# Optimization experiments

Hardware: AMD Instinct MI355X
Metric: run time of the kernel (lower is better)

Reference implementation:

```python
import jax, jax.numpy as jnp
from jax import lax
import numpy as np

B, N = 8192, 4096


def thomas_algorithm(a, b, c, f):
    """Batched Thomas tridiagonal solve.
    a: (B, N-1) sub-diagonal (row i uses a[:, i-1])
    b: (B, N)   diagonal
    c: (B, N-1) super-diagonal (row i uses c[:, i])
    f: (B, N)   rhs
    returns u: (B, N) with A u = f
    """
    Bb = f.shape[0]
    zero_col = jnp.zeros((Bb, 1), dtype=f.dtype)
    a_full = jnp.concatenate([zero_col, a], axis=1)  # (B, N), a_full[:,0] unused (=0)
    c_full = jnp.concatenate([c, zero_col], axis=1)  # (B, N), c_full[:,N-1] unused (=0)

    def fwd_step(carry, inp):
        cp_prev, dp_prev = carry
        ai, bi, ci, fi = inp
        denom = bi - ai * cp_prev
        cp = ci / denom
        dp = (fi - ai * dp_prev) / denom
        return (cp, dp), (cp, dp)

    init = (jnp.zeros(Bb, dtype=f.dtype), jnp.zeros(Bb, dtype=f.dtype))
    xs = (a_full.T, b.T, c_full.T, f.T)  # scan over N, vectorized over B
    _, (cps, dps) = lax.scan(fwd_step, init, xs)

    def bwd_step(u_next, inp):
        cp, dp = inp
        u = dp - cp * u_next
        return u, u

    _, us = lax.scan(bwd_step, jnp.zeros(Bb, dtype=f.dtype), (cps, dps), reverse=True)
    return us.T  # (B, N)


def setup_inputs() -> dict:
    key = jax.random.key(0)
    k1, k2 = jax.random.split(key)
    alpha = jax.random.uniform(k1, (B, N), dtype=jnp.float32)
    f = jax.random.normal(k2, (N,), dtype=jnp.float32)
    return {"alpha": alpha, "f": f}


def reference(alpha, f):
    # f is 1D metadata -> expand to batch, matching torch forward
    f2 = jnp.broadcast_to(f[None, :], alpha.shape)
    # tridiagonal_matrix(alpha)
    a = alpha[:, :-1] ** 2
    b = jnp.maximum(5.0 + alpha ** 3, 0.01)
    c = alpha[:, 1:] ** 2 + 2.0 * alpha[:, 1:]
    u = thomas_algorithm(a, b, c, f2)
    return u
```

## Files before the change

kernel.cpp:

```cpp
#include <hip/hip_runtime.h>


namespace {
constexpr int kN   = 4096;
constexpr int kCH  = 32;
constexpr int kHL  = 8;
constexpr int kR   = kCH + kHL;
constexpr int kNC  = kN / kCH;
constexpr int RPW  = 8;
constexpr int WAVES = 2;
constexpr int THREADS = 64 * WAVES;
constexpr int F4PR = 76;
constexpr int ST4  = 77;
constexpr int APW4 = RPW * ST4;
constexpr int SF4  = 141;
}

__global__ __launch_bounds__(THREADS) void thomas_v7(
    const float4* __restrict__ alpha4,
    const float4* __restrict__ f4,
    float4* __restrict__ u4)
{
  __shared__ float4 sM[WAVES * APW4 + SF4];

  const int bid  = blockIdx.x;
  const int pair = bid & 7;
  const int r0   = (bid >> 3) * (WAVES * RPW);
  const int w    = threadIdx.x >> 6;
  const int lane = threadIdx.x & 63;
  const int rw0  = r0 + w * RPW;
  const int j    = lane & 7;
  const int q    = lane >> 3;

  float4* __restrict__ sA = sM + w * APW4;
  float4* __restrict__ sF = sM + WAVES * APW4;

#define LOAD_TILE(cw, P)                                              \
  {                                                                   \
    const int cb4 = (cw) * 64 - 3;                                    \
    _Pragma("unroll")                                                 \
    for (int it = 0; it < 10; ++it) {                                 \
      int idx = lane + it * 64;                                       \
      if (idx > RPW * F4PR - 1) idx = RPW * F4PR - 1;        \
      const int row = idx / F4PR;                                     \
      const int c4  = idx - row * F4PR;                               \
      int g4 = cb4 + c4;                                              \
      g4 = (g4 < 0) ? 0 : ((g4 > 1023) ? 1023 : g4);   \
      P[it] = alpha4[(size_t)(rw0 + row) * 1024 + g4];                \
    }                                                                 \
  }

#define WRITE_TILE(P)                                                 \
  {                                                                   \
    _Pragma("unroll")                                                 \
    for (int it = 0; it < 10; ++it) {                                 \
      const int idx = lane + it * 64;                                 \
      if (idx < RPW * F4PR) {                                         \
        const int row = idx / F4PR;                                   \
        const int c4  = idx - row * F4PR;                             \
        sA[row * ST4 + c4] = P[it];                                   \
      }                                                               \
    }                                                                 \
  }

#define STEP(am1v, fiv)                                        \
  {                                                            \
    const float c_  = ap1 * (ap1 + 2.0f);                      \
    const float b_  = fmaxf(fmaf(a0 * a0, a0, 5.0f), 0.01f);   \
    const float dn  = fmaf(-c_, ec, b_);                       \
    const float rd  = __builtin_amdgcn_rcpf(dn);               \
    gc = (fiv - c_ * gc) * rd;                                 \
    ec = ((am1v) * (am1v)) * rd;                               \
    ap1 = a0; a0 = (am1v);                                     \
  }

#define SOLVE_TILE(CWL)                                                   \
  {                                                                       \
    const int  kk    = (pair * 2 + (CWL)) * 8 + q;                        \
    const bool first = (kk == 0);                                         \
    const bool last  = (kk == kNC - 1);                                   \
    const int  f4b   = first ? 3 : (q * 8 + 1);                           \
    const int  fOff  = (CWL) * 64;                                        \
    const float4* __restrict__ A4 = sA + j * ST4;                         \
    float gp[kR], ep[kR];                                                 \
    float ec = 0.0f, gc = 0.0f, ap1 = 0.0f;                               \
    const int ghi = last ? 9 : 17;                                        \
    float4 curA = A4[f4b + ghi];                                          \
    float4 lowA = A4[f4b + ghi - 1];                                      \
    float4 fcur = sF[fOff + f4b + ghi];                                   \
    float4 flow = sF[fOff + f4b + ghi - 1];                               \
    float a0 = curA.w;                                                    \
    if (!last) {                                                          \
      _Pragma("unroll")                                                   \
      for (int g = 17; g >= 10; --g) {                                    \
        const float4 pA = A4[f4b + g - 2];                                \
        const float4 pF = sF[fOff + f4b + g - 2];                         \
        STEP(curA.z, fcur.w)                                              \
        STEP(curA.y, fcur.z)                                              \
        STEP(curA.x, fcur.y)                                              \
        STEP(lowA.w, fcur.x)                                              \
        curA = lowA; lowA = pA; fcur = flow; flow = pF;                   \
      }                                                                   \
    }                                                                     \
    _Pragma("unroll")                                                     \
    for (int g = 9; g >= 0; --g) {                                        \
      int pidx = f4b + g - 2;                                             \
      if (pidx < 0) pidx = 0;              \
      const float4 pA = A4[pidx];                                         \
      const float4 pF = sF[fOff + pidx];                                  \
      float lw = lowA.w;                                                  \
      if (g == 0 && first) lw = 0.0f;                        \
      STEP(curA.z, fcur.w)  gp[4*g+3] = gc; ep[4*g+3] = ec;               \
      STEP(curA.y, fcur.z)  gp[4*g+2] = gc; ep[4*g+2] = ec;               \
      STEP(curA.x, fcur.y)  gp[4*g+1] = gc; ep[4*g+1] = ec;               \
      STEP(lw,     fcur.x)  gp[4*g+0] = gc; ep[4*g+0] = ec;               \
      curA = lowA; lowA = pA; fcur = flow; flow = pF;                     \
    }                                                                     \
    const int tmin = first ? 0 : kHL;                                     \
    float up = 0.0f;                                                      \
    float4 pk;                                                            \
    _Pragma("unroll")                                                     \
    for (int t = 0; t < kR; ++t) {                                        \
      const float uv = fmaf(-ep[t], up, gp[t]);                           \
      up = uv;                                                            \
      const int ph = t & 3;                                               \
      if      (ph == 0) pk.x = uv;                                        \
      else if (ph == 1) pk.y = uv;                                        \
      else if (ph == 2) pk.z = uv;                                        \
      else {                                                              \
        pk.w = uv;                                                        \
        if (t - 3 >= tmin && t < tmin + kCH) {                            \
          sA[j * ST4 + q * 8 + ((t - 3 - tmin) >> 2)] = pk;               \
        }                                                                 \
      }                                                                   \
    }                                                                     \
    _Pragma("unroll")                                                     \
    for (int it = 0; it < RPW; ++it) {                                    \
      const float4 v = sA[it * ST4 + lane];                               \
      u4[(size_t)(rw0 + it) * 1024 + (pair * 2 + (CWL)) * 64 + lane] = v; \
    }                                                                     \
  }

  {
    const int fb4 = pair * 128 - 3;
    #pragma unroll
    for (int it = 0; it < 3; ++it) {
      const int idx = lane + it * 64;
      if (idx < 140) {
        int g4 = fb4 + idx;
        g4 = (g4 < 0) ? 0 : ((g4 > 1023) ? 1023 : g4);
        sF[idx] = f4[g4];
      }
    }
  }

  float4 p0[10];
  LOAD_TILE(pair * 2, p0)
  WRITE_TILE(p0)

  float4 p1[10];
  LOAD_TILE(pair * 2 + 1, p1)

  SOLVE_TILE(0)

  WRITE_TILE(p1)

  SOLVE_TILE(1)

#undef LOAD_TILE
#undef WRITE_TILE
#undef STEP
#undef SOLVE_TILE
}

extern "C" void kernel_launch(void* const* d_in, const int* in_sizes, int n_in,
                              void* d_out, int out_size, void* d_ws, size_t ws_size,
                              hipStream_t stream) {
  const float4* alpha = (const float4*)d_in[0];
  const float4* f     = (const float4*)d_in[1];
  float4*       uo    = (float4*)d_out;
  thomas_v7<<<dim3(4096), THREADS, 0, stream>>>(alpha, f, uo);
}
```

Measured before the change: 55.03 us.

## Pipeline tile loads with direct global-to-LDS double buffering per wave

```diff
diff --git a/kernel.cpp b/kernel.cpp
--- a/kernel.cpp
+++ b/kernel.cpp
@@ -2,65 +2,70 @@
 
 
 namespace {
-constexpr int kN   = 4096;
 constexpr int kCH  = 32;
 constexpr int kHL  = 8;
 constexpr int kR   = kCH + kHL;
-constexpr int kNC  = kN / kCH;
 constexpr int RPW  = 8;
-constexpr int WAVES = 2;
-constexpr int THREADS = 64 * WAVES;
 constexpr int F4PR = 76;
-constexpr int ST4  = 77;
-constexpr int APW4 = RPW * ST4;
-constexpr int SF4  = 141;
+constexpr int APAN = RPW * F4PR;
 }
 
-__global__ __launch_bounds__(THREADS) void thomas_v7(
+__device__ __forceinline__ void glds16(const float4* g, float4* l) {
+  __builtin_amdgcn_global_load_lds(
+      (const __attribute__((address_space(1))) unsigned int*)g,
+      (__attribute__((address_space(3))) unsigned int*)l, 16, 0, 0);
+}
+
+__global__ __launch_bounds__(64) void thomas_v8(
     const float4* __restrict__ alpha4,
     const float4* __restrict__ f4,
     float4* __restrict__ u4)
 {
-  __shared__ float4 sM[WAVES * APW4 + SF4];
+  __shared__ float4 sA[2 * APAN];
+  __shared__ float4 sF[2 * F4PR];
 
   const int bid  = blockIdx.x;
-  const int pair = bid & 7;
-  const int r0   = (bid >> 3) * (WAVES * RPW);
-  const int w    = threadIdx.x >> 6;
-  const int lane = threadIdx.x & 63;
-  const int rw0  = r0 + w * RPW;
+  const int half = bid & 1;
+  const int rw0  = (bid >> 1) * RPW;
+  const int lane = threadIdx.x;
   const int j    = lane & 7;
   const int q    = lane >> 3;
 
-  float4* __restrict__ sA = sM + w * APW4;
-  float4* __restrict__ sF = sM + WAVES * APW4;
-
-#define LOAD_TILE(cw, P)                                              \
-  {                                                                   \
-    const int cb4 = (cw) * 64 - 3;                                    \
-    _Pragma("unroll")                                                 \
-    for (int it = 0; it < 10; ++it) {                                 \
-      int idx = lane + it * 64;                                       \
-      if (idx > RPW * F4PR - 1) idx = RPW * F4PR - 1;        \
-      const int row = idx / F4PR;                                     \
-      const int c4  = idx - row * F4PR;                               \
-      int g4 = cb4 + c4;                                              \
-      g4 = (g4 < 0) ? 0 : ((g4 > 1023) ? 1023 : g4);   \
-      P[it] = alpha4[(size_t)(rw0 + row) * 1024 + g4];                \
-    }                                                                 \
+  const float4* rowp[10];
+  int c4t[10];
+  #pragma unroll
+  for (int it = 0; it < 10; ++it) {
+    const int idx = it * 64 + lane;
+    int row = idx / F4PR;
+    if (row > 7) row = 7;
+    c4t[it] = idx - row * F4PR;
+    rowp[it] = alpha4 + (size_t)(rw0 + row) * 1024;
   }
 
-#define WRITE_TILE(P)                                                 \
-  {                                                                   \
-    _Pragma("unroll")                                                 \
-    for (int it = 0; it < 10; ++it) {                                 \
-      const int idx = lane + it * 64;                                 \
-      if (idx < RPW * F4PR) {                                         \
-        const int row = idx / F4PR;                                   \
-        const int c4  = idx - row * F4PR;                             \
-        sA[row * ST4 + c4] = P[it];                                   \
-      }                                                               \
-    }                                                                 \
+#define PREFETCH(TT, AB, FB)                                              \
+  {                                                                       \
+    const int cb4_ = (half * 8 + (TT)) * 64 - 3;                          \
+    _Pragma("unroll")                                                     \
+    for (int it = 0; it < 9; ++it) {                                      \
+      int g4 = cb4_ + c4t[it];                                            \
+      g4 = (g4 < 0) ? 0 : ((g4 > 1023) ? 1023 : g4);     \
+      glds16(rowp[it] + g4, (AB) + it * 64);                              \
+    }                                                                     \
+    if (lane < 32) {                                    \
+      int g4 = cb4_ + c4t[9];                                             \
+      g4 = (g4 < 0) ? 0 : ((g4 > 1023) ? 1023 : g4);                      \
+      glds16(rowp[9] + g4, (AB) + 9 * 64);                                \
+    }                                                                     \
+    {                                                                     \
+      int gf = cb4_ + lane;                                               \
+      gf = (gf < 0) ? 0 : ((gf > 1023) ? 1023 : gf);                      \
+      glds16(f4 + gf, (FB));                                              \
+    }                                                                     \
+    if (lane < 12) {                                                      \
+      int gf = cb4_ + 64 + lane;                                          \
+      gf = (gf > 1023) ? 1023 : gf;                                       \
+      glds16(f4 + gf, (FB) + 64);                                         \
+    }                                                                     \
   }
 
 #define STEP(am1v, fiv)                                        \
@@ -74,27 +79,28 @@
     ap1 = a0; a0 = (am1v);                                     \
   }
 
-#define SOLVE_TILE(CWL)                                                   \
+#define SOLVE_TILE(TT, AB, FB)                                            \
   {                                                                       \
-    const int  kk    = (pair * 2 + (CWL)) * 8 + q;                        \
+    const int  cw_   = half * 8 + (TT);                                   \
+    const int  kk    = cw_ * 8 + q;                                       \
     const bool first = (kk == 0);                                         \
-    const bool last  = (kk == kNC - 1);                                   \
+    const bool last  = (kk == 127);                                       \
     const int  f4b   = first ? 3 : (q * 8 + 1);                           \
-    const int  fOff  = (CWL) * 64;                                        \
-    const float4* __restrict__ A4 = sA + j * ST4;                         \
+    const float4* __restrict__ A4 = (AB) + j * F4PR;                      \
+    const float4* __restrict__ Fb = (FB);                                 \
     float gp[kR], ep[kR];                                                 \
     float ec = 0.0f, gc = 0.0f, ap1 = 0.0f;                               \
     const int ghi = last ? 9 : 17;                                        \
     float4 curA = A4[f4b + ghi];                                          \
     float4 lowA = A4[f4b + ghi - 1];                                      \
-    float4 fcur = sF[fOff + f4b + ghi];                                   \
-    float4 flow = sF[fOff + f4b + ghi - 1];                               \
+    float4 fcur = Fb[f4b + ghi];                                          \
+    float4 flow = Fb[f4b + ghi - 1];                                      \
     float a0 = curA.w;                                                    \
     if (!last) {                                                          \
       _Pragma("unroll")                                                   \
       for (int g = 17; g >= 10; --g) {                                    \
         const float4 pA = A4[f4b + g - 2];                                \
-        const float4 pF = sF[fOff + f4b + g - 2];                         \
+        const float4 pF = Fb[f4b + g - 2];                                \
         STEP(curA.z, fcur.w)                                              \
         STEP(curA.y, fcur.z)                                              \
         STEP(curA.x, fcur.y)                                              \
@@ -107,7 +113,7 @@
       int pidx = f4b + g - 2;                                             \
       if (pidx < 0) pidx = 0;              \
       const float4 pA = A4[pidx];                                         \
-      const float4 pF = sF[fOff + pidx];                                  \
+      const float4 pF = Fb[pidx];                                         \
       float lw = lowA.w;                                                  \
       if (g == 0 && first) lw = 0.0f;                        \
       STEP(curA.z, fcur.w)  gp[4*g+3] = gc; ep[4*g+3] = ec;               \
@@ -120,55 +126,43 @@
     float up = 0.0f;                                                      \
     float4 pk;                                                            \
     _Pragma("unroll")                                                     \
-    for (int t = 0; t < kR; ++t) {                                        \
-      const float uv = fmaf(-ep[t], up, gp[t]);                           \
+    for (int t_ = 0; t_ < kR; ++t_) {                                     \
+      const float uv = fmaf(-ep[t_], up, gp[t_]);                         \
       up = uv;                                                            \
-      const int ph = t & 3;                                               \
+      const int ph = t_ & 3;                                              \
       if      (ph == 0) pk.x = uv;                                        \
       else if (ph == 1) pk.y = uv;                                        \
       else if (ph == 2) pk.z = uv;                                        \
       else {                                                              \
         pk.w = uv;                                                        \
-        if (t - 3 >= tmin && t < tmin + kCH) {                            \
-          sA[j * ST4 + q * 8 + ((t - 3 - tmin) >> 2)] = pk;               \
+        if (t_ - 3 >= tmin && t_ < tmin + kCH) {                          \
+          (AB)[j * F4PR + q * 8 + ((t_ - 3 - tmin) >> 2)] = pk;           \
         }                                                                 \
       }                                                                   \
     }                                                                     \
     _Pragma("unroll")                                                     \
-    for (int it = 0; it < RPW; ++it) {                                    \
-      const float4 v = sA[it * ST4 + lane];                               \
-      u4[(size_t)(rw0 + it) * 1024 + (pair * 2 + (CWL)) * 64 + lane] = v; \
+    for (int rr = 0; rr < RPW; ++rr) {                                    \
+      const float4 v = (AB)[rr * F4PR + lane];                            \
+      u4[(size_t)(rw0 + rr) * 1024 + cw_ * 64 + lane] = v;                \
     }                                                                     \
   }
 
-  {
-    const int fb4 = pair * 128 - 3;
-    #pragma unroll
-    for (int it = 0; it < 3; ++it) {
-      const int idx = lane + it * 64;
-      if (idx < 140) {
-        int g4 = fb4 + idx;
-        g4 = (g4 < 0) ? 0 : ((g4 > 1023) ? 1023 : g4);
-        sF[idx] = f4[g4];
-      }
-    }
+  PREFETCH(0, sA, sF)
+  PREFETCH(1, sA + APAN, sF + F4PR)
+
+  #pragma unroll 1
+  for (int t = 0; t < 8; ++t) {
+    float4* ab = (t & 1) ? (sA + APAN) : sA;
+    float4* fb = (t & 1) ? (sF + F4PR) : sF;
+    if (t == 0)      asm volatile("s_waitcnt vmcnt(12)" ::: "memory");
+    else if (t == 7) asm volatile("s_waitcnt vmcnt(8)"  ::: "memory");
+    else             asm volatile("s_waitcnt vmcnt(20)" ::: "memory");
+    SOLVE_TILE(t, ab, fb)
+    asm volatile("s_waitcnt lgkmcnt(0)" ::: "memory");
+    if (t < 6) PREFETCH(t + 2, ab, fb)
   }
 
-  float4 p0[10];
-  LOAD_TILE(pair * 2, p0)
-  WRITE_TILE(p0)
-
-  float4 p1[10];
-  LOAD_TILE(pair * 2 + 1, p1)
-
-  SOLVE_TILE(0)
-
-  WRITE_TILE(p1)
-
-  SOLVE_TILE(1)
-
-#undef LOAD_TILE
-#undef WRITE_TILE
+#undef PREFETCH
 #undef STEP
 #undef SOLVE_TILE
 }
@@ -179,5 +173,5 @@
   const float4* alpha = (const float4*)d_in[0];
   const float4* f     = (const float4*)d_in[1];
   float4*       uo    = (float4*)d_out;
-  thomas_v7<<<dim3(4096), THREADS, 0, stream>>>(alpha, f, uo);
+  thomas_v8<<<dim3(2048), 64, 0, stream>>>(alpha, f, uo);
 }
```

New measurement: 68.10 us. 23.7% more time.
